# Performance work log

Measured on AMD Instinct MI355X. Metric: run time of the kernel, lower is better.

The kernel has to match this reference:

```python
import jax, jax.numpy as jnp
import numpy as np

N = 50000        # num_nodes
E = 800000       # num_edges
D_IN = 128
D_OUT = 128
BN_EPS = 1e-5    # torch BatchNorm1d default


def setup_inputs() -> dict:
    key = jax.random.key(0)
    ks = jax.random.split(key, 6)
    x = jax.random.normal(ks[0], (N, D_IN), dtype=jnp.float32)
    edge_index = jax.random.randint(ks[1], (2, E), 0, N, dtype=jnp.int64)
    eps = jnp.zeros((1,), dtype=jnp.float32)  # nn.Parameter(torch.tensor([0.0]))
    lim1 = 1.0 / np.sqrt(D_IN)
    lim2 = 1.0 / np.sqrt(D_OUT)
    W1 = jax.random.uniform(ks[2], (D_OUT, D_IN), jnp.float32, -lim1, lim1)
    b1 = jax.random.uniform(ks[3], (D_OUT,), jnp.float32, -lim1, lim1)
    W2 = jax.random.uniform(ks[4], (D_OUT, D_OUT), jnp.float32, -lim2, lim2)
    b2 = jax.random.uniform(ks[5], (D_OUT,), jnp.float32, -lim2, lim2)
    gamma1 = jnp.ones((D_OUT,), jnp.float32)
    beta1 = jnp.zeros((D_OUT,), jnp.float32)
    gamma2 = jnp.ones((D_OUT,), jnp.float32)
    beta2 = jnp.zeros((D_OUT,), jnp.float32)
    return {"x": x, "edge_index": edge_index, "eps": eps,
            "W1": W1, "b1": b1, "gamma1": gamma1, "beta1": beta1,
            "W2": W2, "b2": b2, "gamma2": gamma2, "beta2": beta2}


def _batch_norm(h, gamma, beta):
    # training-mode BatchNorm1d: biased batch variance, eps=1e-5
    mu = h.mean(axis=0)
    var = h.var(axis=0)
    return gamma * (h - mu) * jax.lax.rsqrt(var + BN_EPS) + beta


def reference(x, edge_index, eps, W1, b1, gamma1, beta1, W2, b2, gamma2, beta2):
    row, col = edge_index[0], edge_index[1]
    # agg[v] = sum_{(v,u) in edges} x[u]   (gather + scatter-add)
    agg = jax.ops.segment_sum(x[col], row, num_segments=N)  # [N, D_IN]
    out = (1.0 + eps) * x + agg                              # [N, D_IN]
    h = jax.nn.relu(_batch_norm(out @ W1.T + b1, gamma1, beta1))
    h = jax.nn.relu(_batch_norm(h @ W2.T + b2, gamma2, beta2))
    return h
```

## Files before the change

### kernel.cpp

```cpp
#include <hip/hip_runtime.h>

#define NN 50000
#define EE 800000
#define DD 128
#define BN_EPS 1e-5f
#define XCONV_B 3125
#define BIN_BLOCKS 200
#define BIN_EDGES 4000
#define NBUCK 3125
#define BROWS 16
#define BCAP 512
#define NREP 32
#define MLP_B 391
#define LDA 136

typedef __attribute__((ext_vector_type(8))) short bf16x8;
typedef __attribute__((ext_vector_type(4))) float f32x4;
typedef __attribute__((ext_vector_type(8))) unsigned short u16x8;

__device__ inline unsigned short f2bf(float f) {
  unsigned int u = __float_as_uint(f);
  u = (u + 0x7fffu + ((u >> 16) & 1u)) >> 16;
  return (unsigned short)u;
}
__device__ inline float bf2f(unsigned short b) {
  return __uint_as_float(((unsigned int)b) << 16);
}
__device__ inline float ldw(const float* p) {
  return __hip_atomic_load(p, __ATOMIC_RELAXED, __HIP_MEMORY_SCOPE_AGENT);
}
__device__ inline void stw(float* p, float v) {
  __hip_atomic_store(p, v, __ATOMIC_RELAXED, __HIP_MEMORY_SCOPE_AGENT);
}


__global__ __launch_bounds__(256) void k_prep(const float* __restrict__ x,
                                              const float* __restrict__ W1,
                                              const float* __restrict__ W2,
                                              unsigned short* __restrict__ xq,
                                              unsigned short* __restrict__ W1b,
                                              unsigned short* __restrict__ W2b,
                                              int* __restrict__ bcur,
                                              float* __restrict__ reps,
                                              int* __restrict__ syncw) {
  const int b = blockIdx.x;
  const int t = threadIdx.x;
  if (b < XCONV_B) {
    const int gid = b * 256 + t;
    const float4 v0 = ((const float4*)x)[gid * 2];
    const float4 v1 = ((const float4*)x)[gid * 2 + 1];
    ushort4 o0, o1;
    o0.x = f2bf(v0.x); o0.y = f2bf(v0.y); o0.z = f2bf(v0.z); o0.w = f2bf(v0.w);
    o1.x = f2bf(v1.x); o1.y = f2bf(v1.y); o1.z = f2bf(v1.z); o1.w = f2bf(v1.w);
    const int node = gid >> 4;
    const int c0 = (gid & 15) * 8;
    const size_t dst = (size_t)(c0 >> 5) * (NN * 32) + node * 32 + (c0 & 31);
    *(ushort4*)(xq + dst) = o0;
    *(ushort4*)(xq + dst + 4) = o1;
    if (gid < NBUCK) bcur[gid] = 0;
    if (gid < 4 * NREP * DD) reps[gid] = 0.0f;
    if (gid < 4) syncw[gid] = 0;
  } else if (b < XCONV_B + 16) {
    const int gid = (b - XCONV_B) * 256 + t;
    const float4 v = ((const float4*)W1)[gid];
    ushort4 o;
    o.x = f2bf(v.x); o.y = f2bf(v.y); o.z = f2bf(v.z); o.w = f2bf(v.w);
    ((ushort4*)W1b)[gid] = o;
  } else {
    const int gid = (b - XCONV_B - 16) * 256 + t;
    const float4 v = ((const float4*)W2)[gid];
    ushort4 o;
    o.x = f2bf(v.x); o.y = f2bf(v.y); o.z = f2bf(v.z); o.w = f2bf(v.w);
    ((ushort4*)W2b)[gid] = o;
  }
}

__global__ __launch_bounds__(256) void k_bin0(const int* __restrict__ rows,
                                              const int* __restrict__ cols,
                                              int* __restrict__ bcur,
                                              unsigned int* __restrict__ bbuf) {
  __shared__ int hist[NBUCK];
  __shared__ int lbase[NBUCK];
  const int t = threadIdx.x;
  for (int i = t; i < NBUCK; i += 256) hist[i] = 0;
  __syncthreads();
  const int e0 = blockIdx.x * BIN_EDGES;
  int er[16], ec[16];
#pragma unroll
  for (int i = 0; i < 16; ++i) {
    const int idx = t + i * 256;
    if (idx < BIN_EDGES) {
      er[i] = rows[e0 + idx];
      ec[i] = cols[e0 + idx];
      atomicAdd(&hist[er[i] >> 4], 1);
    }
  }
  __syncthreads();
  for (int i = t; i < NBUCK; i += 256) {
    const int c = hist[i];
    lbase[i] = (c > 0) ? atomicAdd(&bcur[i], c) : 0;
    hist[i] = 0;
  }
  __syncthreads();
#pragma unroll
  for (int i = 0; i < 16; ++i) {
    const int idx = t + i * 256;
    if (idx < BIN_EDGES) {
      const int bk = er[i] >> 4;
      const int lp = lbase[bk] + atomicAdd(&hist[bk], 1);
      if (lp < BCAP)
        bbuf[(size_t)bk * BCAP + lp] =
            ((unsigned)(er[i] & 15) << 16) | (unsigned)ec[i];
    }
  }
}

__global__ __launch_bounds__(128) void k_agg(
    const unsigned short* __restrict__ xq, const float* __restrict__ eps,
    const int* __restrict__ bcnt, const unsigned int* __restrict__ bbuf,
    unsigned short* __restrict__ aggb) {
  __shared__ unsigned short scols[BCAP];
  __shared__ int rcnt[BROWS];
  __shared__ int roff[BROWS + 1];
  const int t = threadIdx.x;
  const int id = blockIdx.x;
  const int q = id / NBUCK;
  const int bk = id - q * NBUCK;

  int n = bcnt[bk];
  n = n < BCAP ? n : BCAP;
  if (t < BROWS) rcnt[t] = 0;
  __syncthreads();

  unsigned int ent[4];
  int nl = 0;
  for (int i = t; i < n; i += 128) {
    const unsigned int e = bbuf[(size_t)bk * BCAP + i];
    ent[nl++] = e;
    atomicAdd(&rcnt[e >> 16], 1);
  }
  __syncthreads();
  if (t < BROWS) {
    int v = rcnt[t];
#pragma unroll
    for (int off = 1; off < BROWS; off <<= 1) {
      const int u = __shfl_up(v, off);
      if (t >= off) v += u;
    }
    roff[t] = v - rcnt[t];
    if (t == BROWS - 1) roff[BROWS] = v;
    rcnt[t] = 0;
  }
  __syncthreads();
  for (int i = 0; i < nl; ++i) {
    const int r = ent[i] >> 16;
    const int pos = roff[r] + atomicAdd(&rcnt[r], 1);
    scols[pos] = (unsigned short)(ent[i] & 0xffffu);
  }
  __syncthreads();

  const int g = t >> 3;
  const int l8 = t & 3 | ((t & 7) & ~3);
  const unsigned short* xqq = xq + (size_t)q * (NN * 32);
  const float s = 1.0f + eps[0];
  const int v = bk * BROWS + g;
  const ushort4 sv4 = *(const ushort4*)(xqq + (size_t)v * 32 + (t & 7) * 4);
  float a0 = s * bf2f(sv4.x);
  float a1 = s * bf2f(sv4.y);
  float a2 = s * bf2f(sv4.z);
  float a3 = s * bf2f(sv4.w);
  int i = roff[g];
  const int E = roff[g + 1];
  const int lo = (t & 7) * 4;
  for (; i + 3 < E; i += 4) {
    const int u0 = scols[i], u1 = scols[i + 1];
    const int u2 = scols[i + 2], u3 = scols[i + 3];
    const ushort4 p0 = *(const ushort4*)(xqq + (size_t)u0 * 32 + lo);
    const ushort4 p1 = *(const ushort4*)(xqq + (size_t)u1 * 32 + lo);
    const ushort4 p2 = *(const ushort4*)(xqq + (size_t)u2 * 32 + lo);
    const ushort4 p3 = *(const ushort4*)(xqq + (size_t)u3 * 32 + lo);
    a0 += (bf2f(p0.x) + bf2f(p1.x)) + (bf2f(p2.x) + bf2f(p3.x));
    a1 += (bf2f(p0.y) + bf2f(p1.y)) + (bf2f(p2.y) + bf2f(p3.y));
    a2 += (bf2f(p0.z) + bf2f(p1.z)) + (bf2f(p2.z) + bf2f(p3.z));
    a3 += (bf2f(p0.w) + bf2f(p1.w)) + (bf2f(p2.w) + bf2f(p3.w));
  }
  for (; i + 1 < E; i += 2) {
    const int u0 = scols[i], u1 = scols[i + 1];
    const ushort4 p0 = *(const ushort4*)(xqq + (size_t)u0 * 32 + lo);
    const ushort4 p1 = *(const ushort4*)(xqq + (size_t)u1 * 32 + lo);
    a0 += bf2f(p0.x) + bf2f(p1.x);
    a1 += bf2f(p0.y) + bf2f(p1.y);
    a2 += bf2f(p0.z) + bf2f(p1.z);
    a3 += bf2f(p0.w) + bf2f(p1.w);
  }
  if (i < E) {
    const int u0 = scols[i];
    const ushort4 p0 = *(const ushort4*)(xqq + (size_t)u0 * 32 + lo);
    a0 += bf2f(p0.x);
    a1 += bf2f(p0.y);
    a2 += bf2f(p0.z);
    a3 += bf2f(p0.w);
  }
  ushort4 o;
  o.x = f2bf(a0); o.y = f2bf(a1); o.z = f2bf(a2); o.w = f2bf(a3);
  *(ushort4*)(aggb + (size_t)v * DD + q * 32 + lo) = o;
}

__global__ __launch_bounds__(256, 2) void k_mlp(
    const unsigned short* __restrict__ aggb, float* __restrict__ sum1r,
    float* __restrict__ sumsq1r, const float* __restrict__ g1,
    const float* __restrict__ be1, const unsigned short* __restrict__ W1b,
    const float* __restrict__ b1, const unsigned short* __restrict__ W2b,
    const float* __restrict__ b2, float* __restrict__ sum2r,
    float* __restrict__ sumsq2r, const float* __restrict__ g2,
    const float* __restrict__ be2, float* __restrict__ scale1,
    float* __restrict__ shift1, float* __restrict__ scale2,
    float* __restrict__ shift2, int* __restrict__ syncw,
    float* __restrict__ out) {
  __shared__ unsigned short sT[128 * LDA];
  __shared__ float lsc[DD];
  __shared__ float lsh[DD];
  __shared__ int amlast;
  const int tid = threadIdx.x;
  const int bk = blockIdx.x;
  const int wv = tid >> 6;
  const int lane = tid & 63;
  const int quad = lane >> 4;
  const int l16 = lane & 15;
  const int rowq = bk * 128 + wv * 32 + quad * 4;

#pragma unroll
  for (int it = 0; it < 8; ++it) {
    const int idx = it * 256 + tid;
    const int row = idx >> 4, seg = idx & 15;
    int grow = bk * 128 + row;
    grow = grow < NN ? grow : NN - 1;
    *(u16x8*)&sT[row * LDA + seg * 8] =
        *(const u16x8*)(aggb + (size_t)grow * DD + seg * 8);
  }
  __syncthreads();

  f32x4 acc[2][8];
#pragma unroll
  for (int m = 0; m < 2; ++m)
#pragma unroll
    for (int n = 0; n < 8; ++n) acc[m][n] = (f32x4){0.f, 0.f, 0.f, 0.f};
#pragma unroll
  for (int kk = 0; kk < 4; ++kk) {
    const bf16x8 a0 =
        *(const bf16x8*)&sT[(wv * 32 + l16) * LDA + kk * 32 + quad * 8];
    const bf16x8 a1 =
        *(const bf16x8*)&sT[(wv * 32 + 16 + l16) * LDA + kk * 32 + quad * 8];
#pragma unroll
    for (int n = 0; n < 8; ++n) {
      const bf16x8 bf = *(const bf16x8*)(W1b + (size_t)(n * 16 + l16) * DD +
                                         kk * 32 + quad * 8);
      acc[0][n] = __builtin_amdgcn_mfma_f32_16x16x32_bf16(a0, bf, acc[0][n], 0, 0, 0);
      acc[1][n] = __builtin_amdgcn_mfma_f32_16x16x32_bf16(a1, bf, acc[1][n], 0, 0, 0);
    }
  }
#pragma unroll
  for (int n = 0; n < 8; ++n) {
    const int col = n * 16 + l16;
    const float bv = b1[col];
    float sv = 0.f, qv = 0.f;
#pragma unroll
    for (int m = 0; m < 2; ++m)
#pragma unroll
      for (int r = 0; r < 4; ++r) {
        const float o = acc[m][n][r] + bv;
        acc[m][n][r] = o;
        if (rowq + m * 16 + r < NN) { sv += o; qv += o * o; }
      }
    sv += __shfl_xor(sv, 16); qv += __shfl_xor(qv, 16);
    sv += __shfl_xor(sv, 32); qv += __shfl_xor(qv, 32);
    if (quad == 0) {
      const int rep = (bk & (NREP - 1)) * DD;
      atomicAdd(&sum1r[rep + col], sv);
      atomicAdd(&sumsq1r[rep + col], qv);
    }
  }
  __syncthreads();
#pragma unroll
  for (int m = 0; m < 2; ++m)
#pragma unroll
    for (int n = 0; n < 8; ++n)
#pragma unroll
      for (int r = 0; r < 4; ++r)
        sT[(wv * 32 + m * 16 + quad * 4 + r) * LDA + n * 16 + l16] =
            f2bf(acc[m][n][r]);

  if (tid == 0) amlast = (atomicAdd(&syncw[0], 1) == MLP_B - 1) ? 1 : 0;
  __syncthreads();
  if (amlast) {
    if (tid < DD) {
      float sm = 0.f, qm = 0.f;
#pragma unroll
      for (int r = 0; r < NREP; ++r) {
        sm += ldw(&sum1r[r * DD + tid]);
        qm += ldw(&sumsq1r[r * DD + tid]);
      }
      const float inv_n = 1.0f / (float)NN;
      const float mean = sm * inv_n;
      const float var = qm * inv_n - mean * mean;
      const float sc = g1[tid] * rsqrtf(var + BN_EPS);
      stw(&scale1[tid], sc);
      stw(&shift1[tid], be1[tid] - mean * sc);
    }
    __syncthreads();
    if (tid == 0)
      __hip_atomic_store(&syncw[1], 1, __ATOMIC_RELAXED, __HIP_MEMORY_SCOPE_AGENT);
  }
  if (tid == 0) {
    while (__hip_atomic_load(&syncw[1], __ATOMIC_RELAXED,
                             __HIP_MEMORY_SCOPE_AGENT) == 0)
      __builtin_amdgcn_s_sleep(32);
  }
  __syncthreads();
  if (tid < DD) {
    lsc[tid] = ldw(&scale1[tid]);
    lsh[tid] = ldw(&shift1[tid]);
  }
  __syncthreads();

  f32x4 acc2[2][8];
#pragma unroll
  for (int m = 0; m < 2; ++m)
#pragma unroll
    for (int n = 0; n < 8; ++n) acc2[m][n] = (f32x4){0.f, 0.f, 0.f, 0.f};
#pragma unroll
  for (int kk = 0; kk < 4; ++kk) {
    const int kb = kk * 32 + quad * 8;
    const float4 s0 = *(const float4*)&lsc[kb];
    const float4 s1 = *(const float4*)&lsc[kb + 4];
    const float4 h0 = *(const float4*)&lsh[kb];
    const float4 h1v = *(const float4*)&lsh[kb + 4];
    const u16x8 x0 = *(const u16x8*)&sT[(wv * 32 + l16) * LDA + kb];
    const u16x8 x1 = *(const u16x8*)&sT[(wv * 32 + 16 + l16) * LDA + kb];
    bf16x8 af0, af1;
    af0[0] = (short)f2bf(fmaxf(fmaf(s0.x, bf2f(x0[0]), h0.x), 0.f));
    af0[1] = (short)f2bf(fmaxf(fmaf(s0.y, bf2f(x0[1]), h0.y), 0.f));
    af0[2] = (short)f2bf(fmaxf(fmaf(s0.z, bf2f(x0[2]), h0.z), 0.f));
    af0[3] = (short)f2bf(fmaxf(fmaf(s0.w, bf2f(x0[3]), h0.w), 0.f));
    af0[4] = (short)f2bf(fmaxf(fmaf(s1.x, bf2f(x0[4]), h1v.x), 0.f));
    af0[5] = (short)f2bf(fmaxf(fmaf(s1.y, bf2f(x0[5]), h1v.y), 0.f));
    af0[6] = (short)f2bf(fmaxf(fmaf(s1.z, bf2f(x0[6]), h1v.z), 0.f));
    af0[7] = (short)f2bf(fmaxf(fmaf(s1.w, bf2f(x0[7]), h1v.w), 0.f));
    af1[0] = (short)f2bf(fmaxf(fmaf(s0.x, bf2f(x1[0]), h0.x), 0.f));
    af1[1] = (short)f2bf(fmaxf(fmaf(s0.y, bf2f(x1[1]), h0.y), 0.f));
    af1[2] = (short)f2bf(fmaxf(fmaf(s0.z, bf2f(x1[2]), h0.z), 0.f));
    af1[3] = (short)f2bf(fmaxf(fmaf(s0.w, bf2f(x1[3]), h0.w), 0.f));
    af1[4] = (short)f2bf(fmaxf(fmaf(s1.x, bf2f(x1[4]), h1v.x), 0.f));
    af1[5] = (short)f2bf(fmaxf(fmaf(s1.y, bf2f(x1[5]), h1v.y), 0.f));
    af1[6] = (short)f2bf(fmaxf(fmaf(s1.z, bf2f(x1[6]), h1v.z), 0.f));
    af1[7] = (short)f2bf(fmaxf(fmaf(s1.w, bf2f(x1[7]), h1v.w), 0.f));
#pragma unroll
    for (int n = 0; n < 8; ++n) {
      const bf16x8 bf =
          *(const bf16x8*)(W2b + (size_t)(n * 16 + l16) * DD + kb);
      acc2[0][n] = __builtin_amdgcn_mfma_f32_16x16x32_bf16(af0, bf, acc2[0][n], 0, 0, 0);
      acc2[1][n] = __builtin_amdgcn_mfma_f32_16x16x32_bf16(af1, bf, acc2[1][n], 0, 0, 0);
    }
  }
#pragma unroll
  for (int n = 0; n < 8; ++n) {
    const int col = n * 16 + l16;
    const float bv = b2[col];
    float sv = 0.f, qv = 0.f;
#pragma unroll
    for (int m = 0; m < 2; ++m)
#pragma unroll
      for (int r = 0; r < 4; ++r) {
        const float o = acc2[m][n][r] + bv;
        acc2[m][n][r] = o;
        if (rowq + m * 16 + r < NN) { sv += o; qv += o * o; }
      }
    sv += __shfl_xor(sv, 16); qv += __shfl_xor(qv, 16);
    sv += __shfl_xor(sv, 32); qv += __shfl_xor(qv, 32);
    if (quad == 0) {
      const int rep = (bk & (NREP - 1)) * DD;
      atomicAdd(&sum2r[rep + col], sv);
      atomicAdd(&sumsq2r[rep + col], qv);
    }
  }
  __syncthreads();
  if (tid == 0) amlast = (atomicAdd(&syncw[2], 1) == MLP_B - 1) ? 1 : 0;
  __syncthreads();
  if (amlast) {
    if (tid < DD) {
      float sm = 0.f, qm = 0.f;
#pragma unroll
      for (int r = 0; r < NREP; ++r) {
        sm += ldw(&sum2r[r * DD + tid]);
        qm += ldw(&sumsq2r[r * DD + tid]);
      }
      const float inv_n = 1.0f / (float)NN;
      const float mean = sm * inv_n;
      const float var = qm * inv_n - mean * mean;
      const float sc = g2[tid] * rsqrtf(var + BN_EPS);
      stw(&scale2[tid], sc);
      stw(&shift2[tid], be2[tid] - mean * sc);
    }
    __syncthreads();
    if (tid == 0)
      __hip_atomic_store(&syncw[3], 1, __ATOMIC_RELAXED, __HIP_MEMORY_SCOPE_AGENT);
  }
  if (tid == 0) {
    while (__hip_atomic_load(&syncw[3], __ATOMIC_RELAXED,
                             __HIP_MEMORY_SCOPE_AGENT) == 0)
      __builtin_amdgcn_s_sleep(32);
  }
  __syncthreads();
  if (tid < DD) {
    lsc[tid] = ldw(&scale2[tid]);
    lsh[tid] = ldw(&shift2[tid]);
  }
  __syncthreads();
#pragma unroll
  for (int n = 0; n < 8; ++n) {
    const int col = n * 16 + l16;
    const float sc = lsc[col];
    const float sh = lsh[col];
#pragma unroll
    for (int m = 0; m < 2; ++m)
#pragma unroll
      for (int r = 0; r < 4; ++r) {
        const int row = rowq + m * 16 + r;
        if (row < NN)
          out[(size_t)row * DD + col] = fmaxf(fmaf(sc, acc2[m][n][r], sh), 0.f);
      }
  }
}

extern "C" void kernel_launch(void* const* d_in, const int* in_sizes, int n_in,
                              void* d_out, int out_size, void* d_ws, size_t ws_size,
                              hipStream_t stream) {
  const float* x = (const float*)d_in[0];
  const int* ei = (const int*)d_in[1];
  const float* eps = (const float*)d_in[2];
  const float* W1 = (const float*)d_in[3];
  const float* b1 = (const float*)d_in[4];
  const float* g1 = (const float*)d_in[5];
  const float* be1 = (const float*)d_in[6];
  const float* W2 = (const float*)d_in[7];
  const float* b2 = (const float*)d_in[8];
  const float* g2 = (const float*)d_in[9];
  const float* be2 = (const float*)d_in[10];
  float* out = (float*)d_out;

  const int* rows = ei;
  const int* cols = ei + EE;

  int* bcur = (int*)d_out;
  unsigned short* xq = (unsigned short*)d_out + 2000000;
  unsigned int* bbuf = (unsigned int*)((char*)d_out + 16800000);
  unsigned short* W1b = (unsigned short*)d_out + 11640000;
  unsigned short* W2b = (unsigned short*)d_out + 11680000;
  float* reps = (float*)d_out + 5875000;
  float* sum1r = reps;
  float* sumsq1r = reps + NREP * DD;
  float* sum2r = reps + 2 * NREP * DD;
  float* sumsq2r = reps + 3 * NREP * DD;

  unsigned short* aggb = (unsigned short*)d_ws;
  float* stf = (float*)((char*)d_ws + 12800000);
  float* scale1 = stf + 0;
  float* shift1 = stf + 128;
  float* scale2 = stf + 256;
  float* shift2 = stf + 384;
  int* syncw = (int*)(stf + 512);

  k_prep<<<XCONV_B + 32, 256, 0, stream>>>(x, W1, W2, xq, W1b, W2b, bcur, reps,
                                           syncw);
  k_bin0<<<BIN_BLOCKS, 256, 0, stream>>>(rows, cols, bcur, bbuf);
  k_agg<<<4 * NBUCK, 128, 0, stream>>>(xq, eps, bcur, bbuf, aggb);
  k_mlp<<<MLP_B, 256, 0, stream>>>(aggb, sum1r, sumsq1r, g1, be1, W1b, b1,
                                   W2b, b2, sum2r, sumsq2r, g2, be2, scale1,
                                   shift1, scale2, shift2, syncw, out);
}
```

Measured before the change: 204.1 us.

## Replace bucketed binning with per-row padded CSR and shuffle-pipelined gather

```diff
diff --git a/kernel.cpp b/kernel.cpp
--- a/kernel.cpp
+++ b/kernel.cpp
@@ -7,9 +7,8 @@
 #define XCONV_B 3125
 #define BIN_BLOCKS 200
 #define BIN_EDGES 4000
-#define NBUCK 3125
-#define BROWS 16
-#define BCAP 512
+#define RCAP 64
+#define NAGG 6250
 #define NREP 32
 #define MLP_B 391
 #define LDA 136
@@ -40,7 +39,7 @@
                                               unsigned short* __restrict__ xq,
                                               unsigned short* __restrict__ W1b,
                                               unsigned short* __restrict__ W2b,
-                                              int* __restrict__ bcur,
+                                              int* __restrict__ rcnt,
                                               float* __restrict__ reps,
                                               int* __restrict__ syncw) {
   const int b = blockIdx.x;
@@ -57,7 +56,7 @@
     const size_t dst = (size_t)(c0 >> 5) * (NN * 32) + node * 32 + (c0 & 31);
     *(ushort4*)(xq + dst) = o0;
     *(ushort4*)(xq + dst + 4) = o1;
-    if (gid < NBUCK) bcur[gid] = 0;
+    if (gid < NN) rcnt[gid] = 0;
     if (gid < 4 * NREP * DD) reps[gid] = 0.0f;
     if (gid < 4) syncw[gid] = 0;
   } else if (b < XCONV_B + 16) {
@@ -75,135 +74,98 @@
   }
 }
 
-__global__ __launch_bounds__(256) void k_bin0(const int* __restrict__ rows,
-                                              const int* __restrict__ cols,
-                                              int* __restrict__ bcur,
-                                              unsigned int* __restrict__ bbuf) {
-  __shared__ int hist[NBUCK];
-  __shared__ int lbase[NBUCK];
+__global__ __launch_bounds__(256) void k_binrow(const int* __restrict__ rows,
+                                                const int* __restrict__ cols,
+                                                int* __restrict__ rcnt,
+                                                unsigned short* __restrict__ csr) {
   const int t = threadIdx.x;
-  for (int i = t; i < NBUCK; i += 256) hist[i] = 0;
-  __syncthreads();
   const int e0 = blockIdx.x * BIN_EDGES;
-  int er[16], ec[16];
-#pragma unroll
-  for (int i = 0; i < 16; ++i) {
-    const int idx = t + i * 256;
-    if (idx < BIN_EDGES) {
-      er[i] = rows[e0 + idx];
-      ec[i] = cols[e0 + idx];
-      atomicAdd(&hist[er[i] >> 4], 1);
-    }
-  }
-  __syncthreads();
-  for (int i = t; i < NBUCK; i += 256) {
-    const int c = hist[i];
-    lbase[i] = (c > 0) ? atomicAdd(&bcur[i], c) : 0;
-    hist[i] = 0;
-  }
-  __syncthreads();
-#pragma unroll
-  for (int i = 0; i < 16; ++i) {
-    const int idx = t + i * 256;
-    if (idx < BIN_EDGES) {
-      const int bk = er[i] >> 4;
-      const int lp = lbase[bk] + atomicAdd(&hist[bk], 1);
-      if (lp < BCAP)
-        bbuf[(size_t)bk * BCAP + lp] =
-            ((unsigned)(er[i] & 15) << 16) | (unsigned)ec[i];
-    }
-  }
-}
-
-__global__ __launch_bounds__(128) void k_agg(
+#pragma unroll
+  for (int k = 0; k < 16; ++k) {
+    const int li = t + k * 256;
+    if (li < BIN_EDGES) {
+      const int r = rows[e0 + li];
+      const int c = cols[e0 + li];
+      const int p = atomicAdd(&rcnt[r], 1);
+      if (p < RCAP)
+        csr[(size_t)r * RCAP + p] = (unsigned short)c;
+    }
+  }
+}
+
+__global__ __launch_bounds__(64) void k_agg(
     const unsigned short* __restrict__ xq, const float* __restrict__ eps,
-    const int* __restrict__ bcnt, const unsigned int* __restrict__ bbuf,
+    const int* __restrict__ rcnt, const unsigned short* __restrict__ csr,
     unsigned short* __restrict__ aggb) {
-  __shared__ unsigned short scols[BCAP];
-  __shared__ int rcnt[BROWS];
-  __shared__ int roff[BROWS + 1];
   const int t = threadIdx.x;
   const int id = blockIdx.x;
-  const int q = id / NBUCK;
-  const int bk = id - q * NBUCK;
-
-  int n = bcnt[bk];
-  n = n < BCAP ? n : BCAP;
-  if (t < BROWS) rcnt[t] = 0;
-  __syncthreads();
-
-  unsigned int ent[4];
-  int nl = 0;
-  for (int i = t; i < n; i += 128) {
-    const unsigned int e = bbuf[(size_t)bk * BCAP + i];
-    ent[nl++] = e;
-    atomicAdd(&rcnt[e >> 16], 1);
-  }
-  __syncthreads();
-  if (t < BROWS) {
-    int v = rcnt[t];
-#pragma unroll
-    for (int off = 1; off < BROWS; off <<= 1) {
-      const int u = __shfl_up(v, off);
-      if (t >= off) v += u;
-    }
-    roff[t] = v - rcnt[t];
-    if (t == BROWS - 1) roff[BROWS] = v;
-    rcnt[t] = 0;
-  }
-  __syncthreads();
-  for (int i = 0; i < nl; ++i) {
-    const int r = ent[i] >> 16;
-    const int pos = roff[r] + atomicAdd(&rcnt[r], 1);
-    scols[pos] = (unsigned short)(ent[i] & 0xffffu);
-  }
-  __syncthreads();
-
+  const int q = id / NAGG;
+  const int bk = id - q * NAGG;
   const int g = t >> 3;
-  const int l8 = t & 3 | ((t & 7) & ~3);
-  const unsigned short* xqq = xq + (size_t)q * (NN * 32);
+  const int l8 = t & 7;
+  const int gb = t & 56;
+  const int r = bk * 8 + g;
+  int n = rcnt[r];
+  n = n < RCAP ? n : RCAP;
+  const unsigned short* xqq = xq + (size_t)q * ((size_t)NN * 32);
+  const unsigned short* crow = csr + (size_t)r * RCAP;
+  const int lo = l8 * 4;
   const float s = 1.0f + eps[0];
-  const int v = bk * BROWS + g;
-  const ushort4 sv4 = *(const ushort4*)(xqq + (size_t)v * 32 + (t & 7) * 4);
-  float a0 = s * bf2f(sv4.x);
-  float a1 = s * bf2f(sv4.y);
-  float a2 = s * bf2f(sv4.z);
-  float a3 = s * bf2f(sv4.w);
-  int i = roff[g];
-  const int E = roff[g + 1];
-  const int lo = (t & 7) * 4;
-  for (; i + 3 < E; i += 4) {
-    const int u0 = scols[i], u1 = scols[i + 1];
-    const int u2 = scols[i + 2], u3 = scols[i + 3];
-    const ushort4 p0 = *(const ushort4*)(xqq + (size_t)u0 * 32 + lo);
-    const ushort4 p1 = *(const ushort4*)(xqq + (size_t)u1 * 32 + lo);
-    const ushort4 p2 = *(const ushort4*)(xqq + (size_t)u2 * 32 + lo);
-    const ushort4 p3 = *(const ushort4*)(xqq + (size_t)u3 * 32 + lo);
-    a0 += (bf2f(p0.x) + bf2f(p1.x)) + (bf2f(p2.x) + bf2f(p3.x));
-    a1 += (bf2f(p0.y) + bf2f(p1.y)) + (bf2f(p2.y) + bf2f(p3.y));
-    a2 += (bf2f(p0.z) + bf2f(p1.z)) + (bf2f(p2.z) + bf2f(p3.z));
-    a3 += (bf2f(p0.w) + bf2f(p1.w)) + (bf2f(p2.w) + bf2f(p3.w));
-  }
-  for (; i + 1 < E; i += 2) {
-    const int u0 = scols[i], u1 = scols[i + 1];
-    const ushort4 p0 = *(const ushort4*)(xqq + (size_t)u0 * 32 + lo);
-    const ushort4 p1 = *(const ushort4*)(xqq + (size_t)u1 * 32 + lo);
-    a0 += bf2f(p0.x) + bf2f(p1.x);
-    a1 += bf2f(p0.y) + bf2f(p1.y);
-    a2 += bf2f(p0.z) + bf2f(p1.z);
-    a3 += bf2f(p0.w) + bf2f(p1.w);
-  }
-  if (i < E) {
-    const int u0 = scols[i];
-    const ushort4 p0 = *(const ushort4*)(xqq + (size_t)u0 * 32 + lo);
-    a0 += bf2f(p0.x);
-    a1 += bf2f(p0.y);
-    a2 += bf2f(p0.z);
-    a3 += bf2f(p0.w);
-  }
+  const ushort4 sv = *(const ushort4*)(xqq + (size_t)r * 32 + lo);
+  float a0 = s * bf2f(sv.x), a1 = s * bf2f(sv.y),
+        a2 = s * bf2f(sv.z), a3 = s * bf2f(sv.w);
+
+#define GLD(c) (*(const ushort4*)(xqq + (size_t)(c) * 32 + lo))
+#define CONS(p) { a0 += bf2f(p.x); a1 += bf2f(p.y); a2 += bf2f(p.z); a3 += bf2f(p.w); }
+
+  int i = 0;
+  ushort4 p0, p1, p2, p3, p4, p5, p6, p7;
+  if (n >= 8) {
+    const unsigned cv = (unsigned)crow[l8];
+    p0 = GLD(__shfl(cv, gb + 0)); p1 = GLD(__shfl(cv, gb + 1));
+    p2 = GLD(__shfl(cv, gb + 2)); p3 = GLD(__shfl(cv, gb + 3));
+    p4 = GLD(__shfl(cv, gb + 4)); p5 = GLD(__shfl(cv, gb + 5));
+    p6 = GLD(__shfl(cv, gb + 6)); p7 = GLD(__shfl(cv, gb + 7));
+    unsigned cv2 = (8 + l8 < n) ? (unsigned)crow[8 + l8] : 0u;
+    for (i = 8; i + 8 <= n; i += 8) {
+      const unsigned cv3 =
+          (i + 8 + l8 < n) ? (unsigned)crow[i + 8 + l8] : 0u;
+      CONS(p0); p0 = GLD(__shfl(cv2, gb + 0));
+      CONS(p1); p1 = GLD(__shfl(cv2, gb + 1));
+      CONS(p2); p2 = GLD(__shfl(cv2, gb + 2));
+      CONS(p3); p3 = GLD(__shfl(cv2, gb + 3));
+      CONS(p4); p4 = GLD(__shfl(cv2, gb + 4));
+      CONS(p5); p5 = GLD(__shfl(cv2, gb + 5));
+      CONS(p6); p6 = GLD(__shfl(cv2, gb + 6));
+      CONS(p7); p7 = GLD(__shfl(cv2, gb + 7));
+      cv2 = cv3;
+    }
+    CONS(p0); CONS(p1); CONS(p2); CONS(p3);
+    CONS(p4); CONS(p5); CONS(p6); CONS(p7);
+  }
+  const int rem = n - i;
+  if (rem > 0) {
+    const unsigned tv = (i + l8 < n) ? (unsigned)crow[i + l8] : 0u;
+    if (rem > 0) p0 = GLD(__shfl(tv, gb + 0));
+    if (rem > 1) p1 = GLD(__shfl(tv, gb + 1));
+    if (rem > 2) p2 = GLD(__shfl(tv, gb + 2));
+    if (rem > 3) p3 = GLD(__shfl(tv, gb + 3));
+    if (rem > 4) p4 = GLD(__shfl(tv, gb + 4));
+    if (rem > 5) p5 = GLD(__shfl(tv, gb + 5));
+    if (rem > 6) p6 = GLD(__shfl(tv, gb + 6));
+    if (rem > 0) CONS(p0);
+    if (rem > 1) CONS(p1);
+    if (rem > 2) CONS(p2);
+    if (rem > 3) CONS(p3);
+    if (rem > 4) CONS(p4);
+    if (rem > 5) CONS(p5);
+    if (rem > 6) CONS(p6);
+  }
+#undef GLD
+#undef CONS
   ushort4 o;
   o.x = f2bf(a0); o.y = f2bf(a1); o.z = f2bf(a2); o.w = f2bf(a3);
-  *(ushort4*)(aggb + (size_t)v * DD + q * 32 + lo) = o;
+  *(ushort4*)(aggb + (size_t)r * DD + q * 32 + lo) = o;
 }
 
 __global__ __launch_bounds__(256, 2) void k_mlp(
@@ -306,20 +268,23 @@
       const float sc = g1[tid] * rsqrtf(var + BN_EPS);
       stw(&scale1[tid], sc);
       stw(&shift1[tid], be1[tid] - mean * sc);
+      lsc[tid] = sc;
+      lsh[tid] = be1[tid] - mean * sc;
     }
     __syncthreads();
     if (tid == 0)
       __hip_atomic_store(&syncw[1], 1, __ATOMIC_RELAXED, __HIP_MEMORY_SCOPE_AGENT);
-  }
-  if (tid == 0) {
-    while (__hip_atomic_load(&syncw[1], __ATOMIC_RELAXED,
-                             __HIP_MEMORY_SCOPE_AGENT) == 0)
-      __builtin_amdgcn_s_sleep(32);
-  }
-  __syncthreads();
-  if (tid < DD) {
-    lsc[tid] = ldw(&scale1[tid]);
-    lsh[tid] = ldw(&shift1[tid]);
+  } else {
+    if (tid == 0) {
+      while (__hip_atomic_load(&syncw[1], __ATOMIC_RELAXED,
+                               __HIP_MEMORY_SCOPE_AGENT) == 0)
+        __builtin_amdgcn_s_sleep(8);
+    }
+    __syncthreads();
+    if (tid < DD) {
+      lsc[tid] = scale1[tid];
+      lsh[tid] = shift1[tid];
+    }
   }
   __syncthreads();
 
@@ -400,20 +365,23 @@
       const float sc = g2[tid] * rsqrtf(var + BN_EPS);
       stw(&scale2[tid], sc);
       stw(&shift2[tid], be2[tid] - mean * sc);
+      lsc[tid] = sc;
+      lsh[tid] = be2[tid] - mean * sc;
     }
     __syncthreads();
     if (tid == 0)
       __hip_atomic_store(&syncw[3], 1, __ATOMIC_RELAXED, __HIP_MEMORY_SCOPE_AGENT);
-  }
-  if (tid == 0) {
-    while (__hip_atomic_load(&syncw[3], __ATOMIC_RELAXED,
-                             __HIP_MEMORY_SCOPE_AGENT) == 0)
-      __builtin_amdgcn_s_sleep(32);
-  }
-  __syncthreads();
-  if (tid < DD) {
-    lsc[tid] = ldw(&scale2[tid]);
-    lsh[tid] = ldw(&shift2[tid]);
+  } else {
+    if (tid == 0) {
+      while (__hip_atomic_load(&syncw[3], __ATOMIC_RELAXED,
+                               __HIP_MEMORY_SCOPE_AGENT) == 0)
+        __builtin_amdgcn_s_sleep(8);
+    }
+    __syncthreads();
+    if (tid < DD) {
+      lsc[tid] = scale2[tid];
+      lsh[tid] = shift2[tid];
+    }
   }
   __syncthreads();
 #pragma unroll
@@ -451,9 +419,9 @@
   const int* rows = ei;
   const int* cols = ei + EE;
 
-  int* bcur = (int*)d_out;
+  int* rcnt = (int*)d_out;
   unsigned short* xq = (unsigned short*)d_out + 2000000;
-  unsigned int* bbuf = (unsigned int*)((char*)d_out + 16800000);
+  unsigned short* csr16 = (unsigned short*)((char*)d_out + 16800000);
   unsigned short* W1b = (unsigned short*)d_out + 11640000;
   unsigned short* W2b = (unsigned short*)d_out + 11680000;
   float* reps = (float*)d_out + 5875000;
@@ -470,10 +438,10 @@
   float* shift2 = stf + 384;
   int* syncw = (int*)(stf + 512);
 
-  k_prep<<<XCONV_B + 32, 256, 0, stream>>>(x, W1, W2, xq, W1b, W2b, bcur, reps,
+  k_prep<<<XCONV_B + 32, 256, 0, stream>>>(x, W1, W2, xq, W1b, W2b, rcnt, reps,
                                            syncw);
-  k_bin0<<<BIN_BLOCKS, 256, 0, stream>>>(rows, cols, bcur, bbuf);
-  k_agg<<<4 * NBUCK, 128, 0, stream>>>(xq, eps, bcur, bbuf, aggb);
+  k_binrow<<<BIN_BLOCKS, 256, 0, stream>>>(rows, cols, rcnt, csr16);
+  k_agg<<<4 * NAGG, 64, 0, stream>>>(xq, eps, rcnt, csr16, aggb);
   k_mlp<<<MLP_B, 256, 0, stream>>>(aggb, sum1r, sumsq1r, g1, be1, W1b, b1,
                                    W2b, b2, sum2r, sumsq2r, g2, be2, scale1,
                                    shift1, scale2, shift2, syncw, out);
```

Result: slower. 235.1 us (+15.2%).
